# Performance work log

Hardware: AMD Instinct MI355X
Metric: run time of the kernel (lower is better)

The kernel has to match this reference:

```python
import jax, jax.numpy as jnp
import numpy as np

D_MODEL = 256
N_LEVELS = 4
N_HEADS = 8
N_POINTS = 4
OFF_DIM = 32
D_HEAD = D_MODEL // N_HEADS
SHAPES = [(64, 64), (32, 32), (16, 16), (8, 8)]  # (H_l, W_l)
LEN_IN = sum(h * w for h, w in SHAPES)  # 5440
N_BATCH = 4
LEN_Q = LEN_IN


def _offset_bias_init():
    # replicates _reset_parameters grid_init for sampling_offsets_bias
    thetas = np.arange(N_HEADS, dtype=np.float32) * (2.0 * np.pi / N_HEADS)
    grid = np.stack([np.cos(thetas), np.sin(thetas)], -1)
    grid = grid / np.abs(grid).max(-1, keepdims=True)
    grid = np.tile(grid[:, None, None, :], (1, N_LEVELS, N_POINTS, 1))
    grid = grid * np.arange(1, N_POINTS + 1, dtype=np.float32)[None, None, :, None]
    return jnp.asarray(grid, jnp.float32)  # (H, L, K, 2)


def setup_inputs() -> dict:
    key = jax.random.key(0)
    ks = jax.random.split(key, 12)
    s = 0.02
    return {
        "query": jax.random.normal(ks[0], (N_BATCH, LEN_Q, D_MODEL), jnp.float32),
        "reference_points": jax.random.uniform(ks[1], (N_BATCH, LEN_Q, N_LEVELS, 2), jnp.float32),
        "input_flatten": jax.random.normal(ks[2], (N_BATCH, LEN_IN, D_MODEL), jnp.float32),
        "input_spatial_shapes": jnp.asarray(SHAPES, jnp.int32),
        "offset_embeds_W": jax.random.normal(ks[3], (N_HEADS * N_LEVELS * N_POINTS * OFF_DIM, D_MODEL), jnp.float32) * s,
        "sampling_offsets_W": jax.random.normal(ks[4], (N_HEADS, N_LEVELS, N_POINTS, OFF_DIM, 2), jnp.float32) * s,
        "sampling_offsets_b": _offset_bias_init(),
        "attn_W": jax.random.normal(ks[5], (N_HEADS, N_LEVELS, N_POINTS, OFF_DIM, 1), jnp.float32) * s,
        "attn_b": jax.random.normal(ks[6], (N_HEADS, N_LEVELS, N_POINTS), jnp.float32) * s,
        "value_W": jax.random.normal(ks[7], (D_MODEL, D_MODEL), jnp.float32) * (1.0 / np.sqrt(D_MODEL)),
        "value_b": jnp.zeros((D_MODEL,), jnp.float32),
        "out_W": jax.random.normal(ks[8], (D_MODEL, D_MODEL), jnp.float32) * (1.0 / np.sqrt(D_MODEL)),
        "out_b": jnp.zeros((D_MODEL,), jnp.float32),
    }


def _bilinear(v, loc, H, W):
    # v: (N, heads, H*W, d_head); loc: (N, Lq, heads, K, 2) in [0,1] (x=width, y=height)
    # matches torch grid_sample(mode=bilinear, padding=zeros, align_corners=False)
    N, Lq, Hh, K, _ = loc.shape
    x = loc[..., 0] * W - 0.5
    y = loc[..., 1] * H - 0.5
    x0 = jnp.floor(x)
    y0 = jnp.floor(y)
    wx = (x - x0).transpose(0, 2, 1, 3).reshape(N, Hh, Lq * K)[..., None]
    wy = (y - y0).transpose(0, 2, 1, 3).reshape(N, Hh, Lq * K)[..., None]
    x0i = x0.astype(jnp.int32)
    y0i = y0.astype(jnp.int32)

    def gather(xi, yi):
        valid = (xi >= 0) & (xi < W) & (yi >= 0) & (yi < H)
        idx = jnp.clip(yi, 0, H - 1) * W + jnp.clip(xi, 0, W - 1)
        idx = idx.transpose(0, 2, 1, 3).reshape(N, Hh, Lq * K)
        g = jnp.take_along_axis(v, idx[..., None], axis=2)  # (N, heads, Lq*K, d)
        m = valid.transpose(0, 2, 1, 3).reshape(N, Hh, Lq * K)
        return g * m[..., None].astype(v.dtype)

    g00 = gather(x0i, y0i)
    g01 = gather(x0i + 1, y0i)
    g10 = gather(x0i, y0i + 1)
    g11 = gather(x0i + 1, y0i + 1)
    out = (g00 * (1 - wx) * (1 - wy) + g01 * wx * (1 - wy)
           + g10 * (1 - wx) * wy + g11 * wx * wy)
    return out.reshape(N, Hh, Lq, K, -1)  # (N, heads, Lq, K, d_head)


def _forward(query, reference_points, input_flatten,
             offset_embeds_W, sampling_offsets_W, sampling_offsets_b,
             attn_W, attn_b, value_W, value_b, out_W, out_b):
    N, Lq, _ = query.shape
    # value projection
    value = input_flatten @ value_W.T + value_b                      # (N, Lin, C)
    value = value.reshape(N, -1, N_HEADS, D_HEAD)                    # (N, Lin, H, d)

    # offset embedding + activation (offset_act_name == 'silu')
    oe = jax.nn.silu(query @ offset_embeds_W.T)                      # (N, Lq, H*L*K*off)
    oe = oe.reshape(N, Lq, N_HEADS, N_LEVELS, N_POINTS, OFF_DIM)

    offs = jnp.einsum('bqhlkd,hlkdc->bqhlkc', oe, sampling_offsets_W) + sampling_offsets_b
    aw = jnp.einsum('bqhlkd,hlkd->bqhlk', oe, attn_W[..., 0]) + attn_b
    aw = jax.nn.softmax(aw.reshape(N, Lq, N_HEADS, N_LEVELS * N_POINTS), axis=-1)
    aw = aw.reshape(N, Lq, N_HEADS, N_LEVELS, N_POINTS)

    # normalize offsets by (W_l, H_l) and add reference points (2-dim branch)
    normalizer = jnp.asarray([[w, h] for h, w in SHAPES], jnp.float32)  # (L, 2)
    loc = reference_points[:, :, None, :, None, :] + offs / normalizer[None, None, None, :, None, :]

    out = jnp.zeros((N, Lq, N_HEADS, D_HEAD), jnp.float32)
    start = 0
    for lvl, (H, W) in enumerate(SHAPES):
        v_l = value[:, start:start + H * W].transpose(0, 2, 1, 3)    # (N, heads, HW, d)
        sampled = _bilinear(v_l, loc[:, :, :, lvl], H, W)            # (N, heads, Lq, K, d)
        out = out + jnp.einsum('bhqkd,bqhk->bqhd', sampled, aw[:, :, :, lvl])
        start += H * W
    out = out.reshape(N, Lq, D_MODEL)
    return out @ out_W.T + out_b


def reference(query, reference_points, input_flatten, input_spatial_shapes,
              offset_embeds_W, sampling_offsets_W, sampling_offsets_b,
              attn_W, attn_b, value_W, value_b, out_W, out_b):
    # input_spatial_shapes matches SHAPES (static pyramid)
    return _forward(query, reference_points, input_flatten,
                    offset_embeds_W, sampling_offsets_W, sampling_offsets_b,
                    attn_W, attn_b, value_W, value_b, out_W, out_b)
```

## Files before the change

kernel.cpp:

```cpp
#include <hip/hip_runtime.h>
#include <hip/hip_bf16.h>

#define NB 4
#define LQ 5440
#define DM 256
#define NH 8
#define NL 4
#define NP 4
#define OFFD 32
#define DH 32
#define MTOT (NB * LQ)
#define OEN (NH * NL * NP * OFFD)
#define NGRP (NH * NL * NP)

typedef __attribute__((ext_vector_type(8))) short bf16x8;
typedef __attribute__((ext_vector_type(4))) float f32x4;
typedef unsigned int u32;

#define GLOAD_LDS16(gp, lp) \
    __builtin_amdgcn_global_load_lds((const __attribute__((address_space(1))) u32*)(gp), \
                                     (__attribute__((address_space(3))) u32*)(lp), 16, 0, 0)

__device__ __forceinline__ float bf2f(unsigned short u) {
    union { unsigned int i; float f; } v; v.i = ((unsigned int)u) << 16; return v.f;
}
__device__ __forceinline__ unsigned short f2bf(float x) {
    u32 u = __float_as_uint(x);
    u = u + 0x7fffu + ((u >> 16) & 1u);
    return (unsigned short)(u >> 16);
}
__device__ __forceinline__ u32 pk2(float a, float b) {
    u32 ua = __float_as_uint(a), ub = __float_as_uint(b);
    ua = ua + 0x7fffu + ((ua >> 16) & 1u);
    ub = ub + 0x7fffu + ((ub >> 16) & 1u);
    return (ua >> 16) | (ub & 0xffff0000u);
}
__device__ __forceinline__ float silu(float x) {
    float e = __expf(-x);
    return x * __builtin_amdgcn_rcpf(1.0f + e);
}

__global__ __launch_bounds__(256) void k_cvt2(
    const float* __restrict__ A, unsigned short* __restrict__ Ao,
    const float* __restrict__ B, unsigned short* __restrict__ Bo, int n4)
{
    int i = blockIdx.x * 256 + threadIdx.x;
    if (i >= n4) return;
    const float* src = blockIdx.y ? B : A;
    unsigned short* dst = blockIdx.y ? Bo : Ao;
    float4 v = *(const float4*)(src + (size_t)i * 4);
    ushort4 o;
    o.x = f2bf(v.x); o.y = f2bf(v.y); o.z = f2bf(v.z); o.w = f2bf(v.w);
    *(ushort4*)(dst + (size_t)i * 4) = o;
}
__global__ __launch_bounds__(256) void k_cvt3(
    const float* __restrict__ A, unsigned short* __restrict__ Ao, int nA4,
    const float* __restrict__ B, unsigned short* __restrict__ Bo, int nB4,
    const float* __restrict__ C, unsigned short* __restrict__ Co, int nC4,
    const float* __restrict__ SW, const float* __restrict__ AW,
    unsigned short* __restrict__ Rb)
{
    int i = blockIdx.x * 256 + threadIdx.x;
    if (blockIdx.y == 3) {
        if (i < 65536) {
            int gg = i >> 9, jo = (i >> 5) & 15, d = i & 31;
            float v = 0.f;
            if (jo == 0)      v = SW[(gg * 32 + d) * 2 + 0];
            else if (jo == 1) v = SW[(gg * 32 + d) * 2 + 1];
            else if (jo == 2) v = AW[gg * 32 + d];
            Rb[i] = f2bf(v);
        }
        return;
    }
    const float* src; unsigned short* dst; int n4;
    if (blockIdx.y == 0)      { src = A; dst = Ao; n4 = nA4; }
    else if (blockIdx.y == 1) { src = B; dst = Bo; n4 = nB4; }
    else                      { src = C; dst = Co; n4 = nC4; }
    if (i >= n4) return;
    float4 v = *(const float4*)(src + (size_t)i * 4);
    ushort4 o;
    o.x = f2bf(v.x); o.y = f2bf(v.y); o.z = f2bf(v.z); o.w = f2bf(v.w);
    *(ushort4*)(dst + (size_t)i * 4) = o;
}


__global__ __launch_bounds__(256) void k_oe_mfma(
    const unsigned short* __restrict__ Qb,
    const unsigned short* __restrict__ Wb,
    const unsigned short* __restrict__ Rb,
    const float* __restrict__ SB,
    const float* __restrict__ AB,
    float* __restrict__ offs_out,
    float* __restrict__ aw_out)
{
    __shared__ short sA[128 * 64];
    __shared__ short sB[128 * 64];
    int tid = threadIdx.x;
    int n0 = blockIdx.x * 128;
    int m0 = blockIdx.y * 128;

    int lane = tid & 63;
    int w = tid >> 6;
    int wA = w >> 1;
    int wB = w & 1;
    int lcol = lane & 15, quad = lane >> 4;

    int srow = tid >> 3;
    int sq = (tid & 7) ^ (srow & 7);
    const short* gA = (const short*)Qb + (size_t)(m0 + srow) * 256 + sq * 8;
    const short* gB = (const short*)Wb + (size_t)(n0 + srow) * 256 + sq * 8;
    short* lA = sA + w * 512;
    short* lB = sB + w * 512;

    f32x4 acc[4][4] = {};

    const short* pq = sA + (wB * 64 + lcol) * 64;
    const short* pw = sB + (wA * 64 + lcol) * 64;
    int rx7 = lcol & 7;
    int qa0 = (quad ^ rx7) * 8;
    int qa1 = ((4 + quad) ^ rx7) * 8;

    for (int kc = 0; kc < 256; kc += 64) {
#pragma unroll
        for (int j = 0; j < 4; j++) {
            GLOAD_LDS16(gA + kc + j * 32 * 256, lA + j * 2048);
            GLOAD_LDS16(gB + kc + j * 32 * 256, lB + j * 2048);
        }
        __syncthreads();
        bf16x8 a[4][2], b[4][2];
#pragma unroll
        for (int i = 0; i < 4; i++) {
            a[i][0] = *(const bf16x8*)(pw + i * 16 * 64 + qa0);
            a[i][1] = *(const bf16x8*)(pw + i * 16 * 64 + qa1);
            b[i][0] = *(const bf16x8*)(pq + i * 16 * 64 + qa0);
            b[i][1] = *(const bf16x8*)(pq + i * 16 * 64 + qa1);
        }
#pragma unroll
        for (int kh = 0; kh < 2; kh++)
#pragma unroll
            for (int i = 0; i < 4; i++)
#pragma unroll
                for (int j = 0; j < 4; j++)
                    acc[i][j] = __builtin_amdgcn_mfma_f32_16x16x32_bf16(
                        a[i][kh], b[j][kh], acc[i][j], 0, 0, 0);
        __syncthreads();
    }

    u32 ps[4][4][2];
#pragma unroll
    for (int i = 0; i < 4; i++)
#pragma unroll
        for (int j = 0; j < 4; j++) {
            ps[i][j][0] = pk2(silu(acc[i][j][0]), silu(acc[i][j][1]));
            ps[i][j][1] = pk2(silu(acc[i][j][2]), silu(acc[i][j][3]));
        }

    int srcbase = (quad & 1) * 32 + lcol;
    bool hi = quad >= 2;
    f32x4 zero = {};
#pragma unroll
    for (int g = 0; g < 2; g++) {
        int gg = (n0 + wA * 64 + g * 32) >> 5;
        bf16x8 afrag = *(const bf16x8*)(Rb + ((size_t)(gg * 16 + lcol) * 32 + quad * 8));
        float sb0 = SB[gg * 2 + 0], sb1 = SB[gg * 2 + 1], ab = AB[gg];
#pragma unroll
        for (int j = 0; j < 4; j++) {
            union { u32 u[4]; bf16x8 v; } bf;
#pragma unroll
            for (int b = 0; b < 2; b++) {
                int s = srcbase + b * 16;
#pragma unroll
                for (int c = 0; c < 2; c++) {
                    u32 x0 = (u32)__shfl((int)ps[2 * g + 0][j][c], s);
                    u32 x1 = (u32)__shfl((int)ps[2 * g + 1][j][c], s);
                    bf.u[b * 2 + c] = hi ? x1 : x0;
                }
            }
            f32x4 d2 = __builtin_amdgcn_mfma_f32_16x16x32_bf16(afrag, bf.v, zero, 0, 0, 0);
            if (quad == 0) {
                int m = m0 + wB * 64 + j * 16 + lcol;
                size_t oi = ((size_t)m * NGRP + gg) * 2;
                offs_out[oi + 0] = d2[0] + sb0;
                offs_out[oi + 1] = d2[1] + sb1;
                aw_out[(size_t)m * NGRP + gg] = d2[2] + ab;
            }
        }
    }
}

__global__ __launch_bounds__(256) void k_value_mfma(
    const unsigned short* __restrict__ Xb,
    const unsigned short* __restrict__ Wvb,
    const float* __restrict__ bias,
    unsigned short* __restrict__ Vtb)
{
    __shared__ short sA[128 * 64];
    __shared__ short sB[128 * 64];
    int tid = threadIdx.x;
    int n0 = blockIdx.x * 128;
    int m0 = blockIdx.y * 128;
    int lane = tid & 63;
    int w = tid >> 6;
    int wA = w >> 1;
    int wB = w & 1;
    int lcol = lane & 15, quad = lane >> 4;

    int srow = tid >> 3;
    int sq = (tid & 7) ^ (srow & 7);
    const short* gA = (const short*)Xb + (size_t)(m0 + srow) * 256 + sq * 8;
    const short* gB = (const short*)Wvb + (size_t)(n0 + srow) * 256 + sq * 8;
    short* lA = sA + w * 512;
    short* lB = sB + w * 512;

    f32x4 acc[4][4] = {};
    const short* px = sA + (wB * 64 + lcol) * 64;
    const short* pw = sB + (wA * 64 + lcol) * 64;
    int rx7 = lcol & 7;
    int qa0 = (quad ^ rx7) * 8;
    int qa1 = ((4 + quad) ^ rx7) * 8;

    for (int kc = 0; kc < 256; kc += 64) {
#pragma unroll
        for (int j = 0; j < 4; j++) {
            GLOAD_LDS16(gA + kc + j * 32 * 256, lA + j * 2048);
            GLOAD_LDS16(gB + kc + j * 32 * 256, lB + j * 2048);
        }
        __syncthreads();
        bf16x8 a[4][2], b[4][2];
#pragma unroll
        for (int i = 0; i < 4; i++) {
            a[i][0] = *(const bf16x8*)(pw + i * 16 * 64 + qa0);
            a[i][1] = *(const bf16x8*)(pw + i * 16 * 64 + qa1);
            b[i][0] = *(const bf16x8*)(px + i * 16 * 64 + qa0);
            b[i][1] = *(const bf16x8*)(px + i * 16 * 64 + qa1);
        }
#pragma unroll
        for (int kh = 0; kh < 2; kh++)
#pragma unroll
            for (int i = 0; i < 4; i++)
#pragma unroll
                for (int j = 0; j < 4; j++)
                    acc[i][j] = __builtin_amdgcn_mfma_f32_16x16x32_bf16(
                        a[i][kh], b[j][kh], acc[i][j], 0, 0, 0);
        __syncthreads();
    }

#pragma unroll
    for (int i = 0; i < 4; i++) {
        int nb4 = n0 + wA * 64 + i * 16 + quad * 4;
        int h = nb4 >> 5, db = nb4 & 31;
        float4 b4 = *(const float4*)&bias[nb4];
#pragma unroll
        for (int j = 0; j < 4; j++) {
            int m = m0 + wB * 64 + j * 16 + lcol;
            int b = m / LQ, q = m - b * LQ;
            u32 lo = pk2(acc[i][j][0] + b4.x, acc[i][j][1] + b4.y);
            u32 hi2 = pk2(acc[i][j][2] + b4.z, acc[i][j][3] + b4.w);
            char* dst = (char*)Vtb + ((((size_t)b * NH + h) * LQ + q) * DH + db) * 2;
            *(uint2*)dst = make_uint2(lo, hi2);
        }
    }
}

__global__ __launch_bounds__(256) void k_out_mfma(
    const unsigned short* __restrict__ Xb,
    const unsigned short* __restrict__ Wob,
    const float* __restrict__ bias,
    float* __restrict__ Out)
{
    __shared__ short sA[128 * 64];
    __shared__ short sB[128 * 64];
    int tid = threadIdx.x;
    int n0 = blockIdx.x * 128;
    int m0 = blockIdx.y * 128;
    int lane = tid & 63;
    int w = tid >> 6;
    int wm = w >> 1, wn = w & 1;
    int lcol = lane & 15, lrow = lane >> 4;

    int srow = tid >> 3;
    int sq = (tid & 7) ^ (srow & 7);
    const short* gA = (const short*)Xb + (size_t)(m0 + srow) * 256 + sq * 8;
    const short* gB = (const short*)Wob + (size_t)(n0 + srow) * 256 + sq * 8;
    short* lA = sA + w * 512;
    short* lB = sB + w * 512;

    f32x4 acc[4][4] = {};
    const short* pa = sA + (wm * 64 + lcol) * 64;
    const short* pb = sB + (wn * 64 + lcol) * 64;
    int rx7 = lcol & 7;
    int qa0 = (lrow ^ rx7) * 8;
    int qa1 = ((4 + lrow) ^ rx7) * 8;

    for (int kc = 0; kc < 256; kc += 64) {
#pragma unroll
        for (int j = 0; j < 4; j++) {
            GLOAD_LDS16(gA + kc + j * 32 * 256, lA + j * 2048);
            GLOAD_LDS16(gB + kc + j * 32 * 256, lB + j * 2048);
        }
        __syncthreads();
        bf16x8 a[4][2], b[4][2];
#pragma unroll
        for (int i = 0; i < 4; i++) {
            a[i][0] = *(const bf16x8*)(pa + i * 16 * 64 + qa0);
            a[i][1] = *(const bf16x8*)(pa + i * 16 * 64 + qa1);
            b[i][0] = *(const bf16x8*)(pb + i * 16 * 64 + qa0);
            b[i][1] = *(const bf16x8*)(pb + i * 16 * 64 + qa1);
        }
#pragma unroll
        for (int kh = 0; kh < 2; kh++)
#pragma unroll
            for (int mi = 0; mi < 4; mi++)
#pragma unroll
                for (int ni = 0; ni < 4; ni++)
                    acc[mi][ni] = __builtin_amdgcn_mfma_f32_16x16x32_bf16(
                        a[mi][kh], b[ni][kh], acc[mi][ni], 0, 0, 0);
        __syncthreads();
    }

#pragma unroll
    for (int mi = 0; mi < 4; mi++) {
#pragma unroll
        for (int ni = 0; ni < 4; ni++) {
            int n = n0 + wn * 64 + ni * 16 + lcol;
            float bn = bias[n];
#pragma unroll
            for (int r = 0; r < 4; r++) {
                int m = m0 + wm * 64 + mi * 16 + lrow * 4 + r;
                Out[(size_t)m * 256 + n] = acc[mi][ni][r] + bn;
            }
        }
    }
}

__global__ __launch_bounds__(256) void k_sample(
    const unsigned short* __restrict__ Vtb,
    const float* __restrict__ refp,
    const float* __restrict__ offs,
    const float* __restrict__ awl,
    unsigned short* __restrict__ atnb)
{
    int tid = threadIdx.x;
    int h = blockIdx.y;
    int m_base = blockIdx.x * 4;
    int wv = tid >> 6, lane = tid & 63;
    int m = m_base + wv;
    __shared__ int2 s_iw[4][16][5];

    if (lane < 16) {
        int idx16 = lane;
        int p = h * 16 + idx16;
        int l = idx16 >> 2;
        float logit = awl[(size_t)m * 128 + p];
        float mx = logit;
#pragma unroll
        for (int off = 1; off < 16; off <<= 1) mx = fmaxf(mx, __shfl_xor(mx, off));
        float e = __expf(logit - mx);
        float s = e;
#pragma unroll
        for (int off = 1; off < 16; off <<= 1) s += __shfl_xor(s, off);
        float prob = e * __builtin_amdgcn_rcpf(s);

        float ox = offs[((size_t)m * 128 + p) * 2 + 0];
        float oy = offs[((size_t)m * 128 + p) * 2 + 1];
        float rx = refp[(size_t)m * 8 + l * 2 + 0];
        float ry = refp[(size_t)m * 8 + l * 2 + 1];
        int Wl = 64 >> l;
        int base = (l == 0) ? 0 : (l == 1) ? 4096 : (l == 2) ? 5120 : 5376;
        float fW = (float)Wl;
        float x = rx * fW + ox - 0.5f;
        float y = ry * fW + oy - 0.5f;
        float x0f = floorf(x), y0f = floorf(y);
        float wx = x - x0f, wy = y - y0f;
        int x0 = (int)x0f, y0 = (int)y0f;
        int xc0 = min(max(x0, 0), Wl - 1), xc1 = min(max(x0 + 1, 0), Wl - 1);
        int yc0 = min(max(y0, 0), Wl - 1), yc1 = min(max(y0 + 1, 0), Wl - 1);
        float vx0 = (x0 >= 0 && x0 < Wl) ? 1.f : 0.f;
        float vx1 = (x0 + 1 >= 0 && x0 + 1 < Wl) ? 1.f : 0.f;
        float vy0 = (y0 >= 0 && y0 < Wl) ? 1.f : 0.f;
        float vy1 = (y0 + 1 >= 0 && y0 + 1 < Wl) ? 1.f : 0.f;
        s_iw[wv][idx16][0] = make_int2((base + yc0 * Wl + xc0) * 64,
                                       __float_as_int(prob * (1.f - wx) * (1.f - wy) * vx0 * vy0));
        s_iw[wv][idx16][1] = make_int2((base + yc0 * Wl + xc1) * 64,
                                       __float_as_int(prob * wx * (1.f - wy) * vx1 * vy0));
        s_iw[wv][idx16][2] = make_int2((base + yc1 * Wl + xc0) * 64,
                                       __float_as_int(prob * (1.f - wx) * wy * vx0 * vy1));
        s_iw[wv][idx16][3] = make_int2((base + yc1 * Wl + xc1) * 64,
                                       __float_as_int(prob * wx * wy * vx1 * vy1));
    }
    __syncthreads();

    int p8 = lane >> 3, seg = lane & 7;
    int b = m / LQ;
    const char* ph = (const char*)(Vtb + ((size_t)b * NH + h) * LQ * DH) + seg * 8;
    float a0 = 0.f, a1 = 0.f, a2 = 0.f, a3 = 0.f;
#pragma unroll
    for (int pg = 0; pg < 2; pg++) {
        int pt = pg * 8 + p8;
#pragma unroll
        for (int c = 0; c < 4; c++) {
            int2 iw = s_iw[wv][pt][c];
            uint2 v = *(const uint2*)(ph + iw.x);
            float wgt = __int_as_float(iw.y);
            a0 += wgt * __uint_as_float(v.x << 16);
            a1 += wgt * __uint_as_float(v.x & 0xffff0000u);
            a2 += wgt * __uint_as_float(v.y << 16);
            a3 += wgt * __uint_as_float(v.y & 0xffff0000u);
        }
    }
#pragma unroll
    for (int off = 8; off <= 32; off <<= 1) {
        a0 += __shfl_xor(a0, off);
        a1 += __shfl_xor(a1, off);
        a2 += __shfl_xor(a2, off);
        a3 += __shfl_xor(a3, off);
    }
    if (p8 == 0) {
        ((uint2*)atnb)[(size_t)m * 64 + h * 8 + seg] =
            make_uint2(pk2(a0, a1), pk2(a2, a3));
    }
}

extern "C" void kernel_launch(void* const* d_in, const int* in_sizes, int n_in,
                              void* d_out, int out_size, void* d_ws, size_t ws_size,
                              hipStream_t stream) {
    const float* query  = (const float*)d_in[0];
    const float* refp   = (const float*)d_in[1];
    const float* inflat = (const float*)d_in[2];
    const float* We  = (const float*)d_in[4];
    const float* SW  = (const float*)d_in[5];
    const float* SB  = (const float*)d_in[6];
    const float* AWw = (const float*)d_in[7];
    const float* ABb = (const float*)d_in[8];
    const float* VW  = (const float*)d_in[9];
    const float* Vb  = (const float*)d_in[10];
    const float* OW  = (const float*)d_in[11];
    const float* Ob  = (const float*)d_in[12];
    float* out = (float*)d_out;

    float* ws = (float*)d_ws;
    unsigned short* Vtb  = (unsigned short*)ws;
    float* offs          = ws + 2785280;
    float* awl           = offs + 5570560;
    unsigned short* Qbf  = (unsigned short*)(awl + 2785280);
    unsigned short* Webf = Qbf + 5570560;
    unsigned short* Xbf  = Webf + 1048576;
    unsigned short* Wvbf = Xbf + 5570560;
    unsigned short* OWbf = Wvbf + 65536;
    unsigned short* Rbf  = OWbf + 65536;
    unsigned short* atnb = Xbf;

    k_cvt2<<<dim3(5440, 2), 256, 0, stream>>>(query, Qbf, inflat, Xbf, MTOT * 256 / 4);
    k_cvt3<<<dim3(1024, 4), 256, 0, stream>>>(We, Webf, OEN * 256 / 4,
                                              VW, Wvbf, 256 * 256 / 4,
                                              OW, OWbf, 256 * 256 / 4,
                                              SW, AWw, Rbf);

    k_value_mfma<<<dim3(2, MTOT / 128), 256, 0, stream>>>(Xbf, Wvbf, Vb, Vtb);

    k_oe_mfma<<<dim3(OEN / 128, MTOT / 128), 256, 0, stream>>>(
        Qbf, Webf, Rbf, SB, ABb, offs, awl);

    k_sample<<<dim3(MTOT / 4, NH), 256, 0, stream>>>(Vtb, refp, offs, awl, atnb);

    k_out_mfma<<<dim3(2, MTOT / 128), 256, 0, stream>>>(atnb, OWbf, Ob, out);
}
```

Baseline: 282.8 us.

## Process 64 queries per block in sampling kernel with vectorized weight setup

The sampling kernel now handles 64 queries per block instead of 4. All 256 threads compute the softmax and bilinear indices, one thread per (query, level), using float4 loads. In the gather phase each thread accumulates all 16 points for a (query, segment) pair, so the cross-lane shuffle reduction is gone. This is meant to raise thread utilisation in the setup phase, which was 16 of 64 lanes, and to cut launch and shuffle overhead. The cost is fewer, longer blocks with serial 64-tap loops and a larger LDS table. Every block in a batch stays in one batch because LQ is divisible by 64.

```diff
diff --git a/kernel.cpp b/kernel.cpp
--- a/kernel.cpp
+++ b/kernel.cpp
@@ -342,80 +342,82 @@
 {
     int tid = threadIdx.x;
     int h = blockIdx.y;
-    int m_base = blockIdx.x * 4;
-    int wv = tid >> 6, lane = tid & 63;
-    int m = m_base + wv;
-    __shared__ int2 s_iw[4][16][5];
-
-    if (lane < 16) {
-        int idx16 = lane;
-        int p = h * 16 + idx16;
-        int l = idx16 >> 2;
-        float logit = awl[(size_t)m * 128 + p];
-        float mx = logit;
-#pragma unroll
-        for (int off = 1; off < 16; off <<= 1) mx = fmaxf(mx, __shfl_xor(mx, off));
-        float e = __expf(logit - mx);
-        float s = e;
-#pragma unroll
-        for (int off = 1; off < 16; off <<= 1) s += __shfl_xor(s, off);
-        float prob = e * __builtin_amdgcn_rcpf(s);
-
-        float ox = offs[((size_t)m * 128 + p) * 2 + 0];
-        float oy = offs[((size_t)m * 128 + p) * 2 + 1];
-        float rx = refp[(size_t)m * 8 + l * 2 + 0];
-        float ry = refp[(size_t)m * 8 + l * 2 + 1];
-        int Wl = 64 >> l;
-        int base = (l == 0) ? 0 : (l == 1) ? 4096 : (l == 2) ? 5120 : 5376;
+    int m_base = blockIdx.x * 64;
+    __shared__ int2 s_iw[64][65];
+
+    {
+        int q = tid >> 2, lev = tid & 3;
+        int m = m_base + q;
+        float4 aw4 = *(const float4*)&awl[(size_t)m * 128 + h * 16 + lev * 4];
+        float4 of0 = *(const float4*)&offs[((size_t)m * 128 + h * 16 + lev * 4) * 2];
+        float4 of1 = *(const float4*)&offs[((size_t)m * 128 + h * 16 + lev * 4) * 2 + 4];
+        float rx = refp[(size_t)m * 8 + lev * 2 + 0];
+        float ry = refp[(size_t)m * 8 + lev * 2 + 1];
+
+        float lg[4] = {aw4.x, aw4.y, aw4.z, aw4.w};
+        float mx = fmaxf(fmaxf(lg[0], lg[1]), fmaxf(lg[2], lg[3]));
+        mx = fmaxf(mx, __shfl_xor(mx, 1));
+        mx = fmaxf(mx, __shfl_xor(mx, 2));
+        float e[4]; float s = 0.f;
+#pragma unroll
+        for (int k = 0; k < 4; k++) { e[k] = __expf(lg[k] - mx); s += e[k]; }
+        s += __shfl_xor(s, 1);
+        s += __shfl_xor(s, 2);
+        float inv = __builtin_amdgcn_rcpf(s);
+
+        int Wl = 64 >> lev;
+        int base = (lev == 0) ? 0 : (lev == 1) ? 4096 : (lev == 2) ? 5120 : 5376;
         float fW = (float)Wl;
-        float x = rx * fW + ox - 0.5f;
-        float y = ry * fW + oy - 0.5f;
-        float x0f = floorf(x), y0f = floorf(y);
-        float wx = x - x0f, wy = y - y0f;
-        int x0 = (int)x0f, y0 = (int)y0f;
-        int xc0 = min(max(x0, 0), Wl - 1), xc1 = min(max(x0 + 1, 0), Wl - 1);
-        int yc0 = min(max(y0, 0), Wl - 1), yc1 = min(max(y0 + 1, 0), Wl - 1);
-        float vx0 = (x0 >= 0 && x0 < Wl) ? 1.f : 0.f;
-        float vx1 = (x0 + 1 >= 0 && x0 + 1 < Wl) ? 1.f : 0.f;
-        float vy0 = (y0 >= 0 && y0 < Wl) ? 1.f : 0.f;
-        float vy1 = (y0 + 1 >= 0 && y0 + 1 < Wl) ? 1.f : 0.f;
-        s_iw[wv][idx16][0] = make_int2((base + yc0 * Wl + xc0) * 64,
-                                       __float_as_int(prob * (1.f - wx) * (1.f - wy) * vx0 * vy0));
-        s_iw[wv][idx16][1] = make_int2((base + yc0 * Wl + xc1) * 64,
-                                       __float_as_int(prob * wx * (1.f - wy) * vx1 * vy0));
-        s_iw[wv][idx16][2] = make_int2((base + yc1 * Wl + xc0) * 64,
-                                       __float_as_int(prob * (1.f - wx) * wy * vx0 * vy1));
-        s_iw[wv][idx16][3] = make_int2((base + yc1 * Wl + xc1) * 64,
-                                       __float_as_int(prob * wx * wy * vx1 * vy1));
+        float oxs[4] = {of0.x, of0.z, of1.x, of1.z};
+        float oys[4] = {of0.y, of0.w, of1.y, of1.w};
+#pragma unroll
+        for (int k = 0; k < 4; k++) {
+            float prob = e[k] * inv;
+            float x = rx * fW + oxs[k] - 0.5f;
+            float y = ry * fW + oys[k] - 0.5f;
+            float x0f = floorf(x), y0f = floorf(y);
+            float wx = x - x0f, wy = y - y0f;
+            int x0 = (int)x0f, y0 = (int)y0f;
+            int xc0 = min(max(x0, 0), Wl - 1), xc1 = min(max(x0 + 1, 0), Wl - 1);
+            int yc0 = min(max(y0, 0), Wl - 1), yc1 = min(max(y0 + 1, 0), Wl - 1);
+            float vx0 = (x0 >= 0 && x0 < Wl) ? 1.f : 0.f;
+            float vx1 = (x0 + 1 >= 0 && x0 + 1 < Wl) ? 1.f : 0.f;
+            float vy0 = (y0 >= 0 && y0 < Wl) ? 1.f : 0.f;
+            float vy1 = (y0 + 1 >= 0 && y0 + 1 < Wl) ? 1.f : 0.f;
+            int pi = (lev * 4 + k) * 4;
+            s_iw[q][pi + 0] = make_int2((base + yc0 * Wl + xc0) * 64,
+                                        __float_as_int(prob * (1.f - wx) * (1.f - wy) * vx0 * vy0));
+            s_iw[q][pi + 1] = make_int2((base + yc0 * Wl + xc1) * 64,
+                                        __float_as_int(prob * wx * (1.f - wy) * vx1 * vy0));
+            s_iw[q][pi + 2] = make_int2((base + yc1 * Wl + xc0) * 64,
+                                        __float_as_int(prob * (1.f - wx) * wy * vx0 * vy1));
+            s_iw[q][pi + 3] = make_int2((base + yc1 * Wl + xc1) * 64,
+                                        __float_as_int(prob * wx * wy * vx1 * vy1));
+        }
     }
     __syncthreads();
 
-    int p8 = lane >> 3, seg = lane & 7;
-    int b = m / LQ;
-    const char* ph = (const char*)(Vtb + ((size_t)b * NH + h) * LQ * DH) + seg * 8;
-    float a0 = 0.f, a1 = 0.f, a2 = 0.f, a3 = 0.f;
-#pragma unroll
-    for (int pg = 0; pg < 2; pg++) {
-        int pt = pg * 8 + p8;
-#pragma unroll
-        for (int c = 0; c < 4; c++) {
-            int2 iw = s_iw[wv][pt][c];
-            uint2 v = *(const uint2*)(ph + iw.x);
-            float wgt = __int_as_float(iw.y);
-            a0 += wgt * __uint_as_float(v.x << 16);
-            a1 += wgt * __uint_as_float(v.x & 0xffff0000u);
-            a2 += wgt * __uint_as_float(v.y << 16);
-            a3 += wgt * __uint_as_float(v.y & 0xffff0000u);
-        }
-    }
-#pragma unroll
-    for (int off = 8; off <= 32; off <<= 1) {
-        a0 += __shfl_xor(a0, off);
-        a1 += __shfl_xor(a1, off);
-        a2 += __shfl_xor(a2, off);
-        a3 += __shfl_xor(a3, off);
-    }
-    if (p8 == 0) {
+    int b = m_base / LQ;
+    const char* plane = (const char*)(Vtb + ((size_t)b * NH + h) * LQ * DH);
+    for (int t = 0; t < 2; t++) {
+        int task = tid + t * 256;
+        int q = task >> 3, seg = task & 7;
+        int m = m_base + q;
+        const char* ph = plane + seg * 8;
+        float a0 = 0.f, a1 = 0.f, a2 = 0.f, a3 = 0.f;
+#pragma unroll 4
+        for (int p = 0; p < 16; p++) {
+#pragma unroll
+            for (int c = 0; c < 4; c++) {
+                int2 iw = s_iw[q][p * 4 + c];
+                uint2 v = *(const uint2*)(ph + iw.x);
+                float wgt = __int_as_float(iw.y);
+                a0 += wgt * __uint_as_float(v.x << 16);
+                a1 += wgt * __uint_as_float(v.x & 0xffff0000u);
+                a2 += wgt * __uint_as_float(v.y << 16);
+                a3 += wgt * __uint_as_float(v.y & 0xffff0000u);
+            }
+        }
         ((uint2*)atnb)[(size_t)m * 64 + h * 8 + seg] =
             make_uint2(pk2(a0, a1), pk2(a2, a3));
     }
@@ -461,7 +463,7 @@
     k_oe_mfma<<<dim3(OEN / 128, MTOT / 128), 256, 0, stream>>>(
         Qbf, Webf, Rbf, SB, ABb, offs, awl);
 
-    k_sample<<<dim3(MTOT / 4, NH), 256, 0, stream>>>(Vtb, refp, offs, awl, atnb);
+    k_sample<<<dim3(MTOT / 64, NH), 256, 0, stream>>>(Vtb, refp, offs, awl, atnb);
 
     k_out_mfma<<<dim3(2, MTOT / 128), 256, 0, stream>>>(atnb, OWbf, Ob, out);
 }
```

Measured after the change: 245.2 us. 1.15x faster.
